# Kernel tuning notes

Hardware: AMD Instinct MI355X
Metric: run time of the kernel (lower is better)

## Reference

```python
import jax, jax.numpy as jnp
import numpy as np

M = 4096  # rows (axis -2), cosine transform axis
N = 4096  # cols (axis -1), sine transform axis


def setup_inputs() -> dict:
    key = jax.random.key(0)
    x = jax.random.normal(key, (M, N), dtype=jnp.float32)
    return {"x": x}


def _cos_basis(n):
    # C[u, p] = cos(pi * (2u+1) * p / (2n))  -- IDXCT basis (no coefficient normalization)
    u = jnp.arange(n, dtype=jnp.float32)
    p = jnp.arange(n, dtype=jnp.float32)
    return jnp.cos(jnp.pi * (2.0 * u[:, None] + 1.0) * p[None, :] / (2.0 * n))


def _sin_basis(n):
    # S[v, q] = sin(pi * (2v+1) * q / (2n))  -- IDXST basis (q=0 column is zero)
    v = jnp.arange(n, dtype=jnp.float32)
    q = jnp.arange(n, dtype=jnp.float32)
    return jnp.sin(jnp.pi * (2.0 * v[:, None] + 1.0) * q[None, :] / (2.0 * n))


def reference(x):
    # idcst2(x) = idxct(idxst(x)^T)^T
    # y_{u,v} = sum_p sum_q x_{p,q} * cos(pi*p*(2u+1)/(2M)) * sin(pi*q*(2v+1)/(2N))
    m, n = x.shape[-2], x.shape[-1]
    C0 = _cos_basis(m).astype(x.dtype)  # [M, M]
    S1 = _sin_basis(n).astype(x.dtype)  # [N, N]
    y = jnp.matmul(x, S1.T)   # IDXST along last axis: [M, N]
    out = jnp.matmul(C0, y)   # IDXCT along axis -2:  [M, N]
    return out
```

## Files before the change

kernel.cpp:

```cpp
#include <hip/hip_runtime.h>


#define NF 4096
#define TWOPI_16384 3.8349519697141029e-4f
#define TWOPI_4096  1.5339807878856412e-3f
#define TWOPI_256   2.4543692606170259e-2f

__device__ __forceinline__ float2 cmul(float2 a, float2 b) {
    return make_float2(a.x * b.x - a.y * b.y, a.x * b.y + a.y * b.x);
}
__device__ __forceinline__ float2 cadd(float2 a, float2 b) {
    return make_float2(a.x + b.x, a.y + b.y);
}
__device__ __forceinline__ float2 csub(float2 a, float2 b) {
    return make_float2(a.x - b.x, a.y - b.y);
}
__device__ __forceinline__ float2 muli(float2 a) {
    return make_float2(-a.y, a.x);
}

__device__ __forceinline__ void fft16(float2 f[16]) {
    float2 s[16];
#pragma unroll
    for (int b = 0; b < 4; ++b) {
        float2 x0 = f[b], x1 = f[b + 4], x2 = f[b + 8], x3 = f[b + 12];
        float2 t0 = cadd(x0, x2), t1 = csub(x0, x2);
        float2 t2 = cadd(x1, x3), t3 = csub(x1, x3);
        s[b]      = cadd(t0, t2);
        s[4 + b]  = cadd(t1, muli(t3));
        s[8 + b]  = csub(t0, t2);
        s[12 + b] = csub(t1, muli(t3));
    }
    const float2 w1 = make_float2(0.92387953251128674f, 0.38268343236508977f);
    const float2 w2 = make_float2(0.70710678118654752f, 0.70710678118654752f);
    const float2 w3 = make_float2(0.38268343236508977f, 0.92387953251128674f);
    const float2 w6 = make_float2(-0.70710678118654752f, 0.70710678118654752f);
    const float2 w9 = make_float2(-0.92387953251128674f, -0.38268343236508977f);
    s[5]  = cmul(s[5], w1);
    s[6]  = cmul(s[6], w2);
    s[7]  = cmul(s[7], w3);
    s[9]  = cmul(s[9], w2);
    s[10] = muli(s[10]);
    s[11] = cmul(s[11], w6);
    s[13] = cmul(s[13], w3);
    s[14] = cmul(s[14], w6);
    s[15] = cmul(s[15], w9);
#pragma unroll
    for (int al = 0; al < 4; ++al) {
        float2 x0 = s[4 * al + 0], x1 = s[4 * al + 1];
        float2 x2 = s[4 * al + 2], x3 = s[4 * al + 3];
        float2 t0 = cadd(x0, x2), t1 = csub(x0, x2);
        float2 t2 = cadd(x1, x3), t3 = csub(x1, x3);
        f[al]      = cadd(t0, t2);
        f[4 + al]  = cadd(t1, muli(t3));
        f[8 + al]  = csub(t0, t2);
        f[12 + al] = csub(t1, muli(t3));
    }
}

__device__ __forceinline__ void fftA_store(float2 r[16], float2* __restrict__ buf,
                                           const int t) {
    fft16(r);
    float sn, cs;
    __sincosf((float)t * TWOPI_4096, &sn, &cs);
    const float2 wb = make_float2(cs, sn);
    float2 w = wb;
#pragma unroll
    for (int k1 = 1; k1 < 16; ++k1) { r[k1] = cmul(r[k1], w); w = cmul(w, wb); }
#pragma unroll
    for (int i = 0; i < 16; ++i) buf[i * 256 + t] = r[i];
}

__device__ __forceinline__ void fft4096_tail(float2* __restrict__ buf, const int t) {
    float2 r[16];
    __syncthreads();
    {
        const int k1 = t >> 4, m2 = t & 15;
        const int base = k1 * 256 + m2;
#pragma unroll
        for (int i = 0; i < 16; ++i) r[i] = buf[base + i * 16];
        fft16(r);
        float sn, cs;
        __sincosf((float)m2 * TWOPI_256, &sn, &cs);
        const float2 wb = make_float2(cs, sn);
        float2 w = wb;
#pragma unroll
        for (int j1 = 1; j1 < 16; ++j1) { r[j1] = cmul(r[j1], w); w = cmul(w, wb); }
        __syncthreads();
        const int bw = k1 * 256 + (m2 ^ k1);
#pragma unroll
        for (int j1 = 0; j1 < 16; ++j1) buf[bw + j1 * 16] = r[j1];
    }
    __syncthreads();
    {
        const int k1 = t & 15;
        const int bc = k1 * 256 + (t >> 4) * 16;
#pragma unroll
        for (int i = 0; i < 16; ++i) r[i] = buf[bc + (i ^ k1)];
        fft16(r);
        __syncthreads();
#pragma unroll
        for (int j2 = 0; j2 < 16; ++j2) buf[j2 * 256 + t] = r[j2];
    }
    __syncthreads();
}

__global__ __launch_bounds__(256) void dst_rows_k(const float* __restrict__ x,
                                                  float* __restrict__ y) {
    __shared__ float2 buf[4096];
    const int t = threadIdx.x;
    const size_t r0 = (size_t)blockIdx.x * 2;
    const float* x0 = x + r0 * NF;
    const float* x1 = x0 + NF;

    float sn, cs;
    __sincosf((float)t * TWOPI_16384, &sn, &cs);
    float2 w = make_float2(0.5f * cs, 0.5f * sn);
    const float2 stp = make_float2(0.99518472667219693f, 0.09801714032956060f);
    float2 r[16];
#pragma unroll
    for (int i = 0; i < 16; ++i) {
        const int k = t + 256 * i;
        float2 ww = make_float2(0.f, 0.f);
        if (k > 0) {
            float re = x0[NF - k] + x1[k];
            float im = x1[NF - k] - x0[k];
            ww = make_float2(re * w.x - im * w.y, re * w.y + im * w.x);
        }
        r[i] = ww;
        w = cmul(w, stp);
    }
    fftA_store(r, buf, t);
    fft4096_tail(buf, t);

    float* y0 = y + r0 * NF;
    float* y1 = y0 + NF;
#pragma unroll
    for (int u = 0; u < 8; ++u) {
        const int n = t + 256 * u;
        float2 vn = buf[n];
        float2 vm = buf[NF - 1 - n];
        ((float2*)y0)[n] = make_float2(vn.x, -vm.x);
        ((float2*)y1)[n] = make_float2(vn.y, -vm.y);
    }
}

__global__ __launch_bounds__(256) void dct_rows_k(const float* __restrict__ yt,
                                                  float* __restrict__ ot) {
    __shared__ float2 buf[4096];
    const int t = threadIdx.x;
    const size_t r0 = (size_t)blockIdx.x * 2;
    const float* t0 = yt + r0 * NF;
    const float* t1 = t0 + NF;
    const float a0h = 0.5f * t0[0];
    const float a1h = 0.5f * t1[0];

    float sn, cs;
    __sincosf((float)t * TWOPI_16384, &sn, &cs);
    float2 w = make_float2(0.5f * cs, 0.5f * sn);
    const float2 stp = make_float2(0.99518472667219693f, 0.09801714032956060f);
    float2 r[16];
#pragma unroll
    for (int i = 0; i < 16; ++i) {
        const int k = t + 256 * i;
        if (k == 0) {
            r[i] = make_float2(a0h, a1h);
        } else {
            float re = t0[k] + t1[NF - k];
            float im = t1[k] - t0[NF - k];
            r[i] = make_float2(re * w.x - im * w.y, re * w.y + im * w.x);
        }
        w = cmul(w, stp);
    }
    fftA_store(r, buf, t);
    fft4096_tail(buf, t);

    float* o0 = ot + r0 * NF;
    float* o1 = o0 + NF;
#pragma unroll
    for (int u = 0; u < 8; ++u) {
        const int n = t + 256 * u;
        float2 vn = buf[n];
        float2 vm = buf[NF - 1 - n];
        ((float2*)o0)[n] = make_float2(vn.x + a0h, vm.x + a0h);
        ((float2*)o1)[n] = make_float2(vn.y + a1h, vm.y + a1h);
    }
}

__global__ __launch_bounds__(256) void transpose_k(const float* __restrict__ in,
                                                   float* __restrict__ out) {
    __shared__ float tile[32][33];
    const int tx = threadIdx.x;
    const int ty = threadIdx.y;
    const int c0 = blockIdx.x * 32;
    const int r0 = blockIdx.y * 32;

    float4 v = *(const float4*)(in + (size_t)(r0 + ty) * NF + c0 + 4 * tx);
    tile[ty][4 * tx + 0] = v.x;
    tile[ty][4 * tx + 1] = v.y;
    tile[ty][4 * tx + 2] = v.z;
    tile[ty][4 * tx + 3] = v.w;
    __syncthreads();

    float4 o;
    o.x = tile[4 * tx + 0][ty];
    o.y = tile[4 * tx + 1][ty];
    o.z = tile[4 * tx + 2][ty];
    o.w = tile[4 * tx + 3][ty];
    *(float4*)(out + (size_t)(c0 + ty) * NF + r0 + 4 * tx) = o;
}

extern "C" void kernel_launch(void* const* d_in, const int* in_sizes, int n_in,
                              void* d_out, int out_size, void* d_ws, size_t ws_size,
                              hipStream_t stream) {
    const float* x = (const float*)d_in[0];
    float* out = (float*)d_out;
    float* y = (float*)d_ws;

    dim3 tgrid(128, 128), tblk(8, 32);

    dst_rows_k<<<2048, 256, 0, stream>>>(x, y);
    transpose_k<<<tgrid, tblk, 0, stream>>>(y, out);
    dct_rows_k<<<2048, 256, 0, stream>>>(out, y);
    transpose_k<<<tgrid, tblk, 0, stream>>>(y, out);
}
```

Before: 181.6 us.

## Replace transpose+row DCT with two-pass column FFT kernels

Drops the two transposes and the row-wise DCT. The column DCT now runs directly on the row-major intermediate as a two-pass 4096-point FFT: a first kernel does a radix-16 stage with twiddles into a float2 scratch buffer, and a second does the remaining 256-point stages in shared memory and writes the output columns. This removes two full-matrix transpose round trips through global memory. In exchange it needs a larger workspace (falls back when ws is too small) and adds strided column accesses plus a full complex intermediate array.

```diff
diff --git a/kernel.cpp b/kernel.cpp
--- a/kernel.cpp
+++ b/kernel.cpp
@@ -145,6 +145,126 @@
     }
 }
 
+__global__ __launch_bounds__(256) void colpass1_k(const float* __restrict__ y,
+                                                  float2* __restrict__ H) {
+    const int tid = threadIdx.x;
+    const int cl = tid & 31;
+    const int sl = tid >> 5;
+    const int bs = blockIdx.x & 15;
+    const int bc = blockIdx.x >> 4;
+    const int cpg = bc * 32 + cl;
+    const int c0 = 2 * cpg;
+    const float2 stp = make_float2(0.99518472667219693f, 0.09801714032956060f);
+
+#pragma unroll
+    for (int ii = 0; ii < 2; ++ii) {
+        const int s = 16 * bs + ii * 8 + sl;
+        float2 f[16];
+        float sn, cs;
+        __sincosf((float)s * TWOPI_16384, &sn, &cs);
+        float2 w = make_float2(0.5f * cs, 0.5f * sn);
+#pragma unroll
+        for (int j = 0; j < 16; ++j) {
+            const int k = j * 256 + s;
+            if (k == 0) {
+                float2 r0v = *(const float2*)(y + c0);
+                f[j] = make_float2(0.5f * r0v.x, 0.5f * r0v.y);
+            } else {
+                float2 A = *(const float2*)(y + (size_t)k * NF + c0);
+                float2 Bm = *(const float2*)(y + (size_t)(NF - k) * NF + c0);
+                float re = A.x + Bm.y;
+                float im = A.y - Bm.x;
+                f[j] = make_float2(re * w.x - im * w.y, re * w.y + im * w.x);
+            }
+            w = cmul(w, stp);
+        }
+        fft16(f);
+        __sincosf((float)s * TWOPI_4096, &sn, &cs);
+        const float2 wb = make_float2(cs, sn);
+        float2 wa = wb;
+#pragma unroll
+        for (int a = 1; a < 16; ++a) { f[a] = cmul(f[a], wa); wa = cmul(wa, wb); }
+#pragma unroll
+        for (int a = 0; a < 16; ++a)
+            H[(size_t)(a * 256 + s) * 2048 + cpg] = f[a];
+    }
+}
+
+__global__ __launch_bounds__(256) void colpass2_k(const float2* __restrict__ H,
+                                                  const float* __restrict__ y,
+                                                  float* __restrict__ out) {
+    __shared__ float2 lds[8192];
+    const int tid = threadIdx.x;
+    const int cp = tid & 15;
+    const int g = tid >> 4;
+    const int ap = blockIdx.x & 7;
+    const int bc = blockIdx.x >> 3;
+    const int cpg = bc * 16 + cp;
+    const int c0 = 2 * cpg;
+    int aabs0 = ap, aabs1 = 15 - ap;
+
+#pragma unroll
+    for (int A = 0; A < 2; ++A) {
+        const int abase = (A ? aabs1 : aabs0) * 256;
+        float2 f[16];
+#pragma unroll
+        for (int s1 = 0; s1 < 16; ++s1)
+            f[s1] = H[(size_t)(abase + 16 * s1 + g) * 2048 + cpg];
+        fft16(f);
+        float sn, cs;
+        __sincosf((float)g * TWOPI_256, &sn, &cs);
+        const float2 wb = make_float2(cs, sn);
+        float2 w = wb;
+#pragma unroll
+        for (int b = 1; b < 16; ++b) { f[b] = cmul(f[b], w); w = cmul(w, wb); }
+#pragma unroll
+        for (int b = 0; b < 16; ++b)
+            lds[((A * 16 + b) * 16 + g) * 16 + cp] = f[b];
+    }
+    __syncthreads();
+
+    float2 v0[16], v1[16];
+    {
+        float2 f[16];
+#pragma unroll
+        for (int s0 = 0; s0 < 16; ++s0) f[s0] = lds[(g * 16 + s0) * 16 + cp];
+        fft16(f);
+#pragma unroll
+        for (int c = 0; c < 16; ++c) v0[c] = f[c];
+#pragma unroll
+        for (int s0 = 0; s0 < 16; ++s0)
+            f[s0] = lds[((16 + g) * 16 + s0) * 16 + cp];
+        fft16(f);
+#pragma unroll
+        for (int c = 0; c < 16; ++c) v1[c] = f[c];
+    }
+    __syncthreads();
+
+#pragma unroll
+    for (int c = 0; c < 16; ++c) {
+        lds[(g + 16 * c) * 16 + cp] = v0[c];
+        lds[(256 + g + 16 * c) * 16 + cp] = v1[c];
+    }
+    __syncthreads();
+
+    float2 h0 = *(const float2*)(y + c0);
+    const float a0h = 0.5f * h0.x, a1h = 0.5f * h0.y;
+    const int aout = g >> 3;
+    const int mh = g & 7;
+    const int na = aout ? aabs1 : aabs0;
+#pragma unroll
+    for (int mi = 0; mi < 16; ++mi) {
+        const int m = mh * 16 + mi;
+        const int n = na + 16 * m;
+        float2 vA = lds[(aout * 256 + m) * 16 + cp];
+        float2 vB = lds[((1 - aout) * 256 + (255 - m)) * 16 + cp];
+        *(float2*)(out + (size_t)(2 * n) * NF + c0) =
+            make_float2(vA.x + a0h, vA.y + a1h);
+        *(float2*)(out + (size_t)(2 * n + 1) * NF + c0) =
+            make_float2(vB.x + a0h, vB.y + a1h);
+    }
+}
+
 __global__ __launch_bounds__(256) void dct_rows_k(const float* __restrict__ yt,
                                                   float* __restrict__ ot) {
     __shared__ float2 buf[4096];
@@ -217,10 +337,16 @@
     float* out = (float*)d_out;
     float* y = (float*)d_ws;
 
-    dim3 tgrid(128, 128), tblk(8, 32);
-
-    dst_rows_k<<<2048, 256, 0, stream>>>(x, y);
-    transpose_k<<<tgrid, tblk, 0, stream>>>(y, out);
-    dct_rows_k<<<2048, 256, 0, stream>>>(out, y);
-    transpose_k<<<tgrid, tblk, 0, stream>>>(y, out);
-}
+    if (ws_size >= ((size_t)128 << 20)) {
+        float2* H = (float2*)(y + ((size_t)64 << 20) / 4);
+        dst_rows_k<<<2048, 256, 0, stream>>>(x, y);
+        colpass1_k<<<1024, 256, 0, stream>>>(y, H);
+        colpass2_k<<<1024, 256, 0, stream>>>(H, y, out);
+    } else {
+        dim3 tgrid(128, 128), tblk(8, 32);
+        dst_rows_k<<<2048, 256, 0, stream>>>(x, y);
+        transpose_k<<<tgrid, tblk, 0, stream>>>(y, out);
+        dct_rows_k<<<tgrid.x * 16, 256, 0, stream>>>(out, y);
+        transpose_k<<<tgrid, tblk, 0, stream>>>(y, out);
+    }
+}
```

Measured after the change: 179.9 us. No clear change (-0.9%).
